# Optimization experiments

Hardware: AMD Instinct MI355X
Metric: run time of the kernel (lower is better)

The kernel has to match this reference:

```python
import jax, jax.numpy as jnp
import numpy as np

D_MODEL = 1024
N_HEADS = 16
D_H = D_MODEL // N_HEADS
B, S = 2, 2048


def setup_inputs() -> dict:
    key = jax.random.key(0)
    ks = jax.random.split(key, 12)
    s = 1.0 / np.sqrt(D_MODEL)
    inp = {
        "Q": jax.random.normal(ks[0], (B, S, D_MODEL), jnp.float32),
        "K": jax.random.normal(ks[1], (B, S, D_MODEL), jnp.float32),
        "V": jax.random.normal(ks[2], (B, S, D_MODEL), jnp.float32),
        # causal mask: True means masked out (matches masked_fill semantics)
        "masked": jnp.broadcast_to(~jnp.tril(jnp.ones((S, S), bool)), (B, S, S)),
        "WQ_w": jax.random.uniform(ks[3], (D_MODEL, D_MODEL), jnp.float32, -s, s),
        "WQ_b": jax.random.uniform(ks[4], (D_MODEL,), jnp.float32, -s, s),
        "WK_w": jax.random.uniform(ks[5], (D_MODEL, D_MODEL), jnp.float32, -s, s),
        "WK_b": jax.random.uniform(ks[6], (D_MODEL,), jnp.float32, -s, s),
        "WV_w": jax.random.uniform(ks[7], (D_MODEL, D_MODEL), jnp.float32, -s, s),
        "WV_b": jax.random.uniform(ks[8], (D_MODEL,), jnp.float32, -s, s),
        "Wo_w": jax.random.uniform(ks[9], (D_MODEL, D_MODEL), jnp.float32, -s, s),
        "Wo_b": jax.random.uniform(ks[10], (D_MODEL,), jnp.float32, -s, s),
    }
    return inp


def reference(Q, K, V, masked, WQ_w, WQ_b, WK_w, WK_b, WV_w, WV_b, Wo_w, Wo_b):
    b = Q.shape[0]
    # torch Linear: y = x @ W^T + b
    def split_heads(x):
        return x.reshape(b, -1, N_HEADS, D_H).transpose(0, 2, 1, 3)  # [B,H,S,d_h]

    q = split_heads(Q @ WQ_w.T + WQ_b)
    k = split_heads(K @ WK_w.T + WK_b)
    v = split_heads(V @ WV_w.T + WV_b)

    scores = jnp.einsum("bhqd,bhkd->bhqk", q, k) / np.sqrt(D_H)
    scores = jnp.where(masked[:, None, :, :], jnp.float32(-1e9), scores)
    attn = jax.nn.softmax(scores, axis=-1)
    ctx = jnp.einsum("bhqk,bhkd->bhqd", attn, v)  # [B,H,S,d_h]
    ctx = ctx.transpose(0, 2, 1, 3).reshape(b, -1, N_HEADS * D_H)
    return ctx @ Wo_w.T + Wo_b
```

## Files before the change

kernel.cpp:

```cpp
#include <hip/hip_runtime.h>
#include <hip/hip_bf16.h>
#include <math.h>


typedef __bf16 bf16_t;
typedef bf16_t bf16x8 __attribute__((ext_vector_type(8)));
typedef bf16_t bf16x4 __attribute__((ext_vector_type(4)));
typedef float f32x4 __attribute__((ext_vector_type(4)));

#define MFMA16(a, b, c) __builtin_amdgcn_mfma_f32_16x16x32_bf16(a, b, c, 0, 0, 0)

constexpr int S_LEN = 2048;
constexpr int DMODEL = 1024;
constexpr int DHEAD = 64;
constexpr int MTOT = 2 * S_LEN;
constexpr size_t NQ = (size_t)MTOT * DMODEL;
constexpr size_t NW = (size_t)DMODEL * DMODEL;
constexpr float ESC = 0.18033688011112042f;

__device__ __forceinline__ void load_lds16(const void* g, void* l) {
  __builtin_amdgcn_global_load_lds((const __attribute__((address_space(1))) void*)g,
                                   (__attribute__((address_space(3))) void*)l, 16, 0, 0);
}

__device__ __forceinline__ void swap32(unsigned& a, unsigned& b) {
#if __has_builtin(__builtin_amdgcn_permlane32_swap)
  auto r = __builtin_amdgcn_permlane32_swap(a, b, false, false);
  a = r[0]; b = r[1];
#else
  asm volatile("s_nop 1\n\tv_permlane32_swap_b32 %0, %1\n\ts_nop 1"
               : "+v"(a), "+v"(b));
#endif
}
__device__ __forceinline__ void swap16(unsigned& a, unsigned& b) {
#if __has_builtin(__builtin_amdgcn_permlane16_swap)
  auto r = __builtin_amdgcn_permlane16_swap(a, b, false, false);
  a = r[0]; b = r[1];
#else
  asm volatile("s_nop 1\n\tv_permlane16_swap_b32 %0, %1\n\ts_nop 1"
               : "+v"(a), "+v"(b));
#endif
}

__device__ __forceinline__ float fexp2(float x) {
#if __has_builtin(__builtin_amdgcn_exp2f)
  return __builtin_amdgcn_exp2f(x);
#else
  float r;
  asm("v_exp_f32 %0, %1\n\ts_nop 1" : "=v"(r) : "v"(x));
  return r;
#endif
}

__global__ __launch_bounds__(256) void convert_w(
    const float* __restrict__ W0, const float* __restrict__ W1,
    const float* __restrict__ W2, const float* __restrict__ W3,
    bf16_t* __restrict__ dst) {
  const size_t i = ((size_t)blockIdx.x * 256 + threadIdx.x) * 4;
  const float* s;
  size_t off = i;
  if (off < NW) { s = W0; }
  else if (off < 2 * NW) { s = W1; off -= NW; }
  else if (off < 3 * NW) { s = W2; off -= 2 * NW; }
  else { s = W3; off -= 3 * NW; }
  const float4 v4 = *(const float4*)(s + off);
  bf16x4 b;
  b[0] = (bf16_t)v4.x; b[1] = (bf16_t)v4.y; b[2] = (bf16_t)v4.z; b[3] = (bf16_t)v4.w;
  *(bf16x4*)(dst + i) = b;
}

__global__ __launch_bounds__(256, 3) void gemm_qkv(const float* __restrict__ Qf,
                                                   const float* __restrict__ Kf,
                                                   const float* __restrict__ Vf,
                                                   const bf16_t* __restrict__ Wbase,
                                                   const float* __restrict__ b0,
                                                   const float* __restrict__ b1,
                                                   const float* __restrict__ b2,
                                                   bf16_t* __restrict__ obase) {
  __shared__ bf16_t As[128 * 64];
  __shared__ bf16_t Ws[128 * 64];
  const int z = blockIdx.z;
  const int bm = blockIdx.x * 128, bn = blockIdx.y * 128;
  const int lane = threadIdx.x & 63, wave = threadIdx.x >> 6;
  const int col = lane & 15, quad = lane >> 4;
  const int wm = (wave >> 1) * 64, wn = (wave & 1) * 64;
  const int srow8 = lane >> 3, g8 = (lane & 7) ^ srow8;

  f32x4 acc[4][4];
#pragma unroll
  for (int i = 0; i < 4; i++)
#pragma unroll
    for (int j = 0; j < 4; j++)
#pragma unroll
      for (int r = 0; r < 4; r++) acc[i][j][r] = 0.f;

  const float* Af = ((z == 0) ? Qf : (z == 1) ? Kf : Vf) + (size_t)bm * 1024;
  const bf16_t* Wb = Wbase + z * NW + (size_t)bn * 1024;
  const float* bias = (z == 0) ? b0 : ((z == 1) ? b1 : b2);
  bf16_t* out = obase + z * NQ;

  f32x4 pre[8];
  auto grloadA = [&](int k0) {
#pragma unroll
    for (int i = 0; i < 4; i++) {
      const int rbase = (i * 4 + wave) * 8;
      const float* src = Af + (size_t)(rbase + srow8) * 1024 + k0 + g8 * 8;
      pre[2 * i] = *(const f32x4*)src;
      pre[2 * i + 1] = *(const f32x4*)(src + 4);
    }
  };

  grloadA(0);
  for (int k0 = 0; k0 < 1024; k0 += 64) {
    __syncthreads();
#pragma unroll
    for (int i = 0; i < 4; i++) {
      const int rbase = (i * 4 + wave) * 8;
      bf16x8 pk;
#pragma unroll
      for (int j = 0; j < 4; j++) {
        pk[j] = (bf16_t)pre[2 * i][j];
        pk[4 + j] = (bf16_t)pre[2 * i + 1][j];
      }
      *(bf16x8*)&As[rbase * 64 + lane * 8] = pk;
      load_lds16(Wb + (size_t)(rbase + srow8) * 1024 + k0 + g8 * 8, Ws + rbase * 64);
    }
    __syncthreads();
    if (k0 + 64 < 1024) grloadA(k0 + 64);
#pragma unroll
    for (int kc = 0; kc < 2; kc++) {
      const int slot = (kc * 4 + quad) ^ (col & 7);
      bf16x8 af[4], wf[4];
#pragma unroll
      for (int i = 0; i < 4; i++) af[i] = *(const bf16x8*)&As[(wm + i * 16 + col) * 64 + slot * 8];
#pragma unroll
      for (int j = 0; j < 4; j++) wf[j] = *(const bf16x8*)&Ws[(wn + j * 16 + col) * 64 + slot * 8];
#pragma unroll
      for (int i = 0; i < 4; i++)
#pragma unroll
        for (int j = 0; j < 4; j++) acc[i][j] = MFMA16(af[i], wf[j], acc[i][j]);
    }
  }

  const float esc = (z == 0) ? ESC : 1.0f;
#pragma unroll
  for (int i = 0; i < 4; i++) {
#pragma unroll
    for (int j = 0; j < 4; j++) {
      const int n = bn + wn + j * 16 + col;
      const float bv = bias[n];
      const int h = n >> 6, dh = n & 63;
      if (z < 2) {
#pragma unroll
        for (int r = 0; r < 4; r++) {
          const int m = bm + wm + i * 16 + quad * 4 + r;
          const int b = m >> 11, s = m & 2047;
          out[((size_t)((b * 16 + h) * S_LEN + s) << 6) | dh] =
              (bf16_t)((acc[i][j][r] + bv) * esc);
        }
      } else {
        const int m0 = bm + wm + i * 16 + quad * 4;
        const int b = m0 >> 11, s0 = m0 & 2047;
        bf16x4 p4;
#pragma unroll
        for (int r = 0; r < 4; r++) p4[r] = (bf16_t)(acc[i][j][r] + bv);
        *(bf16x4*)&out[(((size_t)((b * 16 + h) * DHEAD + dh)) << 11) | s0] = p4;
      }
    }
  }
}

__global__ __launch_bounds__(256, 2) void gemm_out(const bf16_t* __restrict__ A,
                                                   const float* __restrict__ pO,
                                                   const float* __restrict__ pL,
                                                   const bf16_t* __restrict__ W,
                                                   const float* __restrict__ bias,
                                                   float* __restrict__ out) {
  __shared__ bf16_t As[64 * 64];
  __shared__ bf16_t Ws[128 * 64];
  const int bm = blockIdx.x * 64, bn = blockIdx.y * 128;
  const int lane = threadIdx.x & 63, wave = threadIdx.x >> 6;
  const int col = lane & 15, quad = lane >> 4;
  const int wm = (wave >> 1) * 32, wn = (wave & 1) * 64;
  const int srow = lane >> 3, s7 = lane & 7;
  const int g = s7 ^ srow;

  const int tq = (bm >> 7) & 15;
  const bool isB = (tq >= 8);
  const int p = isB ? (15 - tq) : tq;
  const int b = bm >> 11;
  const int lr0 = (0 * 4 + wave) * 8 + srow;
  const int lr1 = (1 * 4 + wave) * 8 + srow;
  const int rt0 = (bm & 64) + lr0;
  const int rt1 = (bm & 64) + lr1;

  f32x4 acc[2][4];
#pragma unroll
  for (int i = 0; i < 2; i++)
#pragma unroll
    for (int j = 0; j < 4; j++)
#pragma unroll
      for (int r = 0; r < 4; r++) acc[i][j][r] = 0.f;

  const bf16_t* Ab = A + (size_t)bm * 1024;
  const bf16_t* Wb = W + (size_t)bn * 1024;

  f32x4 preO[8];
  float preL[4];
  auto grloadO = [&](int k0) {
    const int h = k0 >> 6;
    const int pair = (b * 16 + h) * 8 + p;
    const float* O0 = pO + (size_t)(pair * 2 + 0) * (128 * 64);
    const float* O1 = pO + (size_t)(pair * 2 + 1) * (128 * 64);
    const float* L0 = pL + (pair * 2 + 0) * 128;
    const float* L1 = pL + (pair * 2 + 1) * 128;
    preO[0] = *(const f32x4*)&O0[rt0 * 64 + g * 8];
    preO[1] = *(const f32x4*)&O0[rt0 * 64 + g * 8 + 4];
    preO[2] = *(const f32x4*)&O1[rt0 * 64 + g * 8];
    preO[3] = *(const f32x4*)&O1[rt0 * 64 + g * 8 + 4];
    preO[4] = *(const f32x4*)&O0[rt1 * 64 + g * 8];
    preO[5] = *(const f32x4*)&O0[rt1 * 64 + g * 8 + 4];
    preO[6] = *(const f32x4*)&O1[rt1 * 64 + g * 8];
    preO[7] = *(const f32x4*)&O1[rt1 * 64 + g * 8 + 4];
    preL[0] = L0[rt0]; preL[1] = L1[rt0];
    preL[2] = L0[rt1]; preL[3] = L1[rt1];
  };
  auto writeAB = [&]() {
#pragma unroll
    for (int i = 0; i < 2; i++) {
      const float inv = 1.f / (preL[2 * i] + preL[2 * i + 1]);
      bf16x8 pk;
#pragma unroll
      for (int j = 0; j < 4; j++) {
        pk[j] = (bf16_t)((preO[4 * i][j] + preO[4 * i + 2][j]) * inv);
        pk[4 + j] = (bf16_t)((preO[4 * i + 1][j] + preO[4 * i + 3][j]) * inv);
      }
      *(bf16x8*)&As[(i * 4 + wave) * 8 * 64 + lane * 8] = pk;
    }
  };

  if (isB) grloadO(0);
  for (int k0 = 0; k0 < 1024; k0 += 64) {
    __syncthreads();
    if (isB) {
      writeAB();
    } else {
#pragma unroll
      for (int i = 0; i < 2; i++) {
        const int rbase = (i * 4 + wave) * 8;
        load_lds16(Ab + (size_t)(rbase + srow) * 1024 + k0 + g * 8, As + rbase * 64);
      }
    }
#pragma unroll
    for (int i = 0; i < 4; i++) {
      const int rbase = (i * 4 + wave) * 8;
      load_lds16(Wb + (size_t)(rbase + srow) * 1024 + k0 + g * 8, Ws + rbase * 64);
    }
    __syncthreads();
    if (isB && k0 + 64 < 1024) grloadO(k0 + 64);
#pragma unroll
    for (int kc = 0; kc < 2; kc++) {
      const int slot = (kc * 4 + quad) ^ (col & 7);
      bf16x8 af[2], wf[4];
#pragma unroll
      for (int i = 0; i < 2; i++) af[i] = *(const bf16x8*)&As[(wm + i * 16 + col) * 64 + slot * 8];
#pragma unroll
      for (int j = 0; j < 4; j++) wf[j] = *(const bf16x8*)&Ws[(wn + j * 16 + col) * 64 + slot * 8];
#pragma unroll
      for (int i = 0; i < 2; i++)
#pragma unroll
        for (int j = 0; j < 4; j++) acc[i][j] = MFMA16(af[i], wf[j], acc[i][j]);
    }
  }

#pragma unroll
  for (int i = 0; i < 2; i++)
#pragma unroll
    for (int j = 0; j < 4; j++) {
      const int n = bn + wn + j * 16 + col;
      const float bv = bias[n];
#pragma unroll
      for (int r = 0; r < 4; r++) {
        const int m = bm + wm + i * 16 + quad * 4 + r;
        out[(size_t)m * DMODEL + n] = acc[i][j][r] + bv;
      }
    }
}

__global__ __launch_bounds__(256, 2) void attn(const bf16_t* __restrict__ q,
                                               const bf16_t* __restrict__ k,
                                               const bf16_t* __restrict__ vT,
                                               bf16_t* __restrict__ ctx,
                                               float* __restrict__ pO,
                                               float* __restrict__ pL) {
  const int bh = blockIdx.x;
  const int p = blockIdx.y;
  const int s = blockIdx.z;
  const int tB = 15 - p;
  const int nA = s ? 0 : (2 * p + 2);
  const int cB0 = s ? (15 - 2 * p) : 0;
  const int lane = threadIdx.x & 63, wave = threadIdx.x >> 6;
  const int col = lane & 15, quad = lane >> 4;
  const int qrel = wave * 16 + col;

  __shared__ bf16_t Ks[2][64 * 64];
  __shared__ bf16_t Vs[2][64 * 64];

  const bf16_t* kbh = k + (size_t)bh * S_LEN * DHEAD;
  const bf16_t* vbh = vT + (size_t)bh * DHEAD * S_LEN;

  const int srow8 = lane >> 3, s7 = lane & 7;
  const int g8 = s7 ^ srow8;

  auto stage = [&](int c, int b) {
#pragma unroll
    for (int i = 0; i < 2; i++) {
      const int rbase = (i * 4 + wave) * 8;
      load_lds16(kbh + (size_t)(c * 64 + rbase + srow8) * DHEAD + g8 * 8,
                 &Ks[b][rbase * 64]);
    }
#pragma unroll
    for (int i = 0; i < 2; i++) {
      const int dbase = (i * 4 + wave) * 8;
      load_lds16(vbh + (size_t)(dbase + srow8) * S_LEN + c * 64 + g8 * 8,
                 &Vs[b][dbase * 64]);
    }
  };

  bf16x8 aqw[2][2];
  f32x4 o0[4], o1[4], lacc0, lacc1;
  const f32x4 Zv = {0.f, 0.f, 0.f, 0.f};

  auto setup = [&](int tile_) {
    const int tq = tile_ ? tB : p;
    const bf16_t* qb = q + ((size_t)bh * S_LEN + tq * 128 + qrel) * DHEAD;
    aqw[0][0] = *(const bf16x8*)(qb + quad * 8);
    aqw[0][1] = *(const bf16x8*)(qb + 32 + quad * 8);
    aqw[1][0] = *(const bf16x8*)(qb + (size_t)64 * DHEAD + quad * 8);
    aqw[1][1] = *(const bf16x8*)(qb + (size_t)64 * DHEAD + 32 + quad * 8);
#pragma unroll
    for (int r = 0; r < 4; r++) { lacc0[r] = 0.f; lacc1[r] = 0.f; }
#pragma unroll
    for (int db = 0; db < 4; db++)
#pragma unroll
      for (int r = 0; r < 4; r++) { o0[db][r] = 0.f; o1[db][r] = 0.f; }
  };

  auto expw = [&](const f32x4& sv, int nb, bool dmask, f32x4& lac,
                  unsigned& w0, unsigned& w1) {
    union { bf16x4 v; unsigned u[2]; } pw;
#pragma unroll
    for (int r = 0; r < 4; r++) {
      float pv = fexp2(sv[r]);
      if (dmask && (nb * 16 + quad * 4 + r) > qrel) pv = 0.f;
      lac[r] += pv;
      pw.v[r] = (bf16_t)pv;
    }
    w0 = pw.u[0]; w1 = pw.u[1];
  };

  stage(cB0, 0);
  int buf = 0;

#pragma unroll 1
  for (int i = 0; i < 17; ++i) {
    const bool inB = (i >= nA);
    const int c = inB ? (cB0 + i - nA) : i;
    const int cm = inB ? (2 * tB + 1) : (2 * p + 1);

    if (i == 0) setup(inB ? 1 : 0);
    else if (i == nA) setup(1);

    __syncthreads();

    if (i < 16) {
      const int i1 = i + 1;
      const int c1 = (i1 < nA) ? i1 : (cB0 + i1 - nA);
      stage(c1, buf ^ 1);
    }

    const bool skip0 = (c == cm);
    const bool mask0 = (c == cm - 1);
    const bool mask1 = (c == cm);

    f32x4 s0[4], s1[4];
    {
      const int sl = quad ^ (col & 7);
      bf16x8 kf[4];
#pragma unroll
      for (int nb = 0; nb < 4; nb++)
        kf[nb] = *(const bf16x8*)&Ks[buf][(nb * 16 + col) * 64 + sl * 8];
      __builtin_amdgcn_s_setprio(1);
      if (!skip0) {
#pragma unroll
        for (int nb = 0; nb < 4; nb++) s0[nb] = MFMA16(kf[nb], aqw[0][0], Zv);
      }
#pragma unroll
      for (int nb = 0; nb < 4; nb++) s1[nb] = MFMA16(kf[nb], aqw[1][0], Zv);
      __builtin_amdgcn_s_setprio(0);
    }
    {
      const int sl = (4 + quad) ^ (col & 7);
      bf16x8 kf[4];
#pragma unroll
      for (int nb = 0; nb < 4; nb++)
        kf[nb] = *(const bf16x8*)&Ks[buf][(nb * 16 + col) * 64 + sl * 8];
      __builtin_amdgcn_s_setprio(1);
      if (!skip0) {
#pragma unroll
        for (int nb = 0; nb < 4; nb++) s0[nb] = MFMA16(kf[nb], aqw[0][1], s0[nb]);
      }
#pragma unroll
      for (int nb = 0; nb < 4; nb++) s1[nb] = MFMA16(kf[nb], aqw[1][1], s1[nb]);
      __builtin_amdgcn_s_setprio(0);
    }

#pragma unroll
    for (int kcp = 0; kcp < 2; kcp++) {
      const int sl = (kcp * 4 + quad) ^ (col & 7);
      bf16x8 bv[4];
#pragma unroll
      for (int db = 0; db < 4; db++)
        bv[db] = *(const bf16x8*)&Vs[buf][(db * 16 + col) * 64 + sl * 8];

      union { unsigned u[4]; bf16x8 v; } pa1, pa0;
      {
        unsigned X0, X1, Y0, Y1;
        expw(s1[2 * kcp], 2 * kcp, mask1, lacc1, X0, X1);
        expw(s1[2 * kcp + 1], 2 * kcp + 1, mask1, lacc1, Y0, Y1);
        swap32(X0, Y0); swap16(X0, Y0);
        swap32(X1, Y1); swap16(X1, Y1);
        pa1.u[0] = X0; pa1.u[1] = X1; pa1.u[2] = Y0; pa1.u[3] = Y1;
      }
      if (!skip0) {
        unsigned X0, X1, Y0, Y1;
        expw(s0[2 * kcp], 2 * kcp, mask0, lacc0, X0, X1);
        expw(s0[2 * kcp + 1], 2 * kcp + 1, mask0, lacc0, Y0, Y1);
        swap32(X0, Y0); swap16(X0, Y0);
        swap32(X1, Y1); swap16(X1, Y1);
        pa0.u[0] = X0; pa0.u[1] = X1; pa0.u[2] = Y0; pa0.u[3] = Y1;
      }
      __builtin_amdgcn_s_setprio(1);
      if (!skip0) {
#pragma unroll
        for (int db = 0; db < 4; db++) o0[db] = MFMA16(bv[db], pa0.v, o0[db]);
      }
#pragma unroll
      for (int db = 0; db < 4; db++) o1[db] = MFMA16(bv[db], pa1.v, o1[db]);
      __builtin_amdgcn_s_setprio(0);
    }

    if (i == nA - 1) {
      float l0 = lacc0[0] + lacc0[1] + lacc0[2] + lacc0[3];
      l0 += __shfl_xor(l0, 16); l0 += __shfl_xor(l0, 32);
      float l1 = lacc1[0] + lacc1[1] + lacc1[2] + lacc1[3];
      l1 += __shfl_xor(l1, 16); l1 += __shfl_xor(l1, 32);
      const float inv0 = 1.f / l0, inv1 = 1.f / l1;
      const int b = bh >> 4, h = bh & 15;
      bf16_t* cb0 = ctx + ((size_t)(b * S_LEN + p * 128 + qrel)) * DMODEL + h * DHEAD;
      bf16_t* cb1 = cb0 + (size_t)64 * DMODEL;
#pragma unroll
      for (int db = 0; db < 4; db++) {
        bf16x4 w0, w1;
#pragma unroll
        for (int r = 0; r < 4; r++) {
          w0[r] = (bf16_t)(o0[db][r] * inv0);
          w1[r] = (bf16_t)(o1[db][r] * inv1);
        }
        *(bf16x4*)&cb0[db * 16 + quad * 4] = w0;
        *(bf16x4*)&cb1[db * 16 + quad * 4] = w1;
      }
    }
    buf ^= 1;
  }

  float l0 = lacc0[0] + lacc0[1] + lacc0[2] + lacc0[3];
  l0 += __shfl_xor(l0, 16); l0 += __shfl_xor(l0, 32);
  float l1 = lacc1[0] + lacc1[1] + lacc1[2] + lacc1[3];
  l1 += __shfl_xor(l1, 16); l1 += __shfl_xor(l1, 32);
  const int slot = ((bh * 8 + p) << 1) | s;
  float* myO = pO + (size_t)slot * (128 * 64);
  float* myL = pL + slot * 128;
#pragma unroll
  for (int db = 0; db < 4; db++) {
    *(f32x4*)&myO[(size_t)qrel * 64 + db * 16 + quad * 4] = o0[db];
    *(f32x4*)&myO[(size_t)(64 + qrel) * 64 + db * 16 + quad * 4] = o1[db];
  }
  if (quad == 0) { myL[qrel] = l0; myL[64 + qrel] = l1; }
}

extern "C" void kernel_launch(void* const* d_in, const int* in_sizes, int n_in,
                              void* d_out, int out_size, void* d_ws, size_t ws_size,
                              hipStream_t stream) {
  const float* Q = (const float*)d_in[0];
  const float* K = (const float*)d_in[1];
  const float* V = (const float*)d_in[2];
  const float* WQw = (const float*)d_in[4];
  const float* WQb = (const float*)d_in[5];
  const float* WKw = (const float*)d_in[6];
  const float* WKb = (const float*)d_in[7];
  const float* WVw = (const float*)d_in[8];
  const float* WVb = (const float*)d_in[9];
  const float* Wow = (const float*)d_in[10];
  const float* Wob = (const float*)d_in[11];

  bf16_t* base = (bf16_t*)d_ws;
  bf16_t* Wc = base + 3 * NQ;
  bf16_t* qp = base + 3 * NQ + 4 * NW;
  bf16_t* ctx = base;
  float* pO = (float*)(base + NQ);
  float* pL = (float*)(Wc + NW / 2);

  convert_w<<<dim3((unsigned)(4 * NW / 4 / 256)), dim3(256), 0, stream>>>(
      WQw, WKw, WVw, Wow, Wc);

  gemm_qkv<<<dim3(32, 8, 3), dim3(256), 0, stream>>>(Q, K, V, Wc, WQb, WKb, WVb, qp);
  attn<<<dim3(32, 8, 2), dim3(256), 0, stream>>>(qp, qp + NQ, qp + 2 * NQ, ctx, pO, pL);
  gemm_out<<<dim3(64, 8), dim3(256), 0, stream>>>(ctx, pO, pL, Wc + 3 * NW, Wob,
                                                  (float*)d_out);
}
```

Baseline: 225.7 us.

## Fuse fp32-to-bf16 weight conversion into GEMM loaders, drop convert kernel

Removes the separate convert_w kernel and has gemm_qkv and gemm_out load fp32 weights directly, converting them to bf16 in registers before writing to LDS. This cuts one kernel launch and the extra write and read of the bf16 weight copy. In exchange, each GEMM block reads fp32 weights (twice the bytes) and repeats the conversion, and the async global-to-LDS path for W becomes register staging with more VGPR pressure. It also adds s_setprio around the MFMA bursts.

```diff
diff --git a/kernel.cpp b/kernel.cpp
--- a/kernel.cpp
+++ b/kernel.cpp
@@ -52,27 +52,12 @@
 #endif
 }
 
-__global__ __launch_bounds__(256) void convert_w(
-    const float* __restrict__ W0, const float* __restrict__ W1,
-    const float* __restrict__ W2, const float* __restrict__ W3,
-    bf16_t* __restrict__ dst) {
-  const size_t i = ((size_t)blockIdx.x * 256 + threadIdx.x) * 4;
-  const float* s;
-  size_t off = i;
-  if (off < NW) { s = W0; }
-  else if (off < 2 * NW) { s = W1; off -= NW; }
-  else if (off < 3 * NW) { s = W2; off -= 2 * NW; }
-  else { s = W3; off -= 3 * NW; }
-  const float4 v4 = *(const float4*)(s + off);
-  bf16x4 b;
-  b[0] = (bf16_t)v4.x; b[1] = (bf16_t)v4.y; b[2] = (bf16_t)v4.z; b[3] = (bf16_t)v4.w;
-  *(bf16x4*)(dst + i) = b;
-}
-
 __global__ __launch_bounds__(256, 3) void gemm_qkv(const float* __restrict__ Qf,
                                                    const float* __restrict__ Kf,
                                                    const float* __restrict__ Vf,
-                                                   const bf16_t* __restrict__ Wbase,
+                                                   const float* __restrict__ W0,
+                                                   const float* __restrict__ W1,
+                                                   const float* __restrict__ W2,
                                                    const float* __restrict__ b0,
                                                    const float* __restrict__ b1,
                                                    const float* __restrict__ b2,
@@ -95,38 +80,46 @@
       for (int r = 0; r < 4; r++) acc[i][j][r] = 0.f;
 
   const float* Af = ((z == 0) ? Qf : (z == 1) ? Kf : Vf) + (size_t)bm * 1024;
-  const bf16_t* Wb = Wbase + z * NW + (size_t)bn * 1024;
+  const float* Wf = ((z == 0) ? W0 : (z == 1) ? W1 : W2) + (size_t)bn * 1024;
   const float* bias = (z == 0) ? b0 : ((z == 1) ? b1 : b2);
   bf16_t* out = obase + z * NQ;
 
-  f32x4 pre[8];
-  auto grloadA = [&](int k0) {
+  f32x4 preA[8], preW[8];
+  auto grload = [&](int k0) {
 #pragma unroll
     for (int i = 0; i < 4; i++) {
       const int rbase = (i * 4 + wave) * 8;
-      const float* src = Af + (size_t)(rbase + srow8) * 1024 + k0 + g8 * 8;
-      pre[2 * i] = *(const f32x4*)src;
-      pre[2 * i + 1] = *(const f32x4*)(src + 4);
-    }
-  };
-
-  grloadA(0);
+      const float* sa = Af + (size_t)(rbase + srow8) * 1024 + k0 + g8 * 8;
+      const float* sw = Wf + (size_t)(rbase + srow8) * 1024 + k0 + g8 * 8;
+      preA[2 * i] = *(const f32x4*)sa;
+      preA[2 * i + 1] = *(const f32x4*)(sa + 4);
+      preW[2 * i] = *(const f32x4*)sw;
+      preW[2 * i + 1] = *(const f32x4*)(sw + 4);
+    }
+  };
+  auto writeAW = [&]() {
+#pragma unroll
+    for (int i = 0; i < 4; i++) {
+      const int rbase = (i * 4 + wave) * 8;
+      bf16x8 pa, pw;
+#pragma unroll
+      for (int j = 0; j < 4; j++) {
+        pa[j] = (bf16_t)preA[2 * i][j];
+        pa[4 + j] = (bf16_t)preA[2 * i + 1][j];
+        pw[j] = (bf16_t)preW[2 * i][j];
+        pw[4 + j] = (bf16_t)preW[2 * i + 1][j];
+      }
+      *(bf16x8*)&As[rbase * 64 + lane * 8] = pa;
+      *(bf16x8*)&Ws[rbase * 64 + lane * 8] = pw;
+    }
+  };
+
+  grload(0);
   for (int k0 = 0; k0 < 1024; k0 += 64) {
     __syncthreads();
-#pragma unroll
-    for (int i = 0; i < 4; i++) {
-      const int rbase = (i * 4 + wave) * 8;
-      bf16x8 pk;
-#pragma unroll
-      for (int j = 0; j < 4; j++) {
-        pk[j] = (bf16_t)pre[2 * i][j];
-        pk[4 + j] = (bf16_t)pre[2 * i + 1][j];
-      }
-      *(bf16x8*)&As[rbase * 64 + lane * 8] = pk;
-      load_lds16(Wb + (size_t)(rbase + srow8) * 1024 + k0 + g8 * 8, Ws + rbase * 64);
-    }
+    writeAW();
     __syncthreads();
-    if (k0 + 64 < 1024) grloadA(k0 + 64);
+    if (k0 + 64 < 1024) grload(k0 + 64);
 #pragma unroll
     for (int kc = 0; kc < 2; kc++) {
       const int slot = (kc * 4 + quad) ^ (col & 7);
@@ -135,10 +128,12 @@
       for (int i = 0; i < 4; i++) af[i] = *(const bf16x8*)&As[(wm + i * 16 + col) * 64 + slot * 8];
 #pragma unroll
       for (int j = 0; j < 4; j++) wf[j] = *(const bf16x8*)&Ws[(wn + j * 16 + col) * 64 + slot * 8];
+      __builtin_amdgcn_s_setprio(1);
 #pragma unroll
       for (int i = 0; i < 4; i++)
 #pragma unroll
         for (int j = 0; j < 4; j++) acc[i][j] = MFMA16(af[i], wf[j], acc[i][j]);
+      __builtin_amdgcn_s_setprio(0);
     }
   }
 
@@ -173,7 +168,7 @@
 __global__ __launch_bounds__(256, 2) void gemm_out(const bf16_t* __restrict__ A,
                                                    const float* __restrict__ pO,
                                                    const float* __restrict__ pL,
-                                                   const bf16_t* __restrict__ W,
+                                                   const float* __restrict__ Wf,
                                                    const float* __restrict__ bias,
                                                    float* __restrict__ out) {
   __shared__ bf16_t As[64 * 64];
@@ -203,10 +198,28 @@
       for (int r = 0; r < 4; r++) acc[i][j][r] = 0.f;
 
   const bf16_t* Ab = A + (size_t)bm * 1024;
-  const bf16_t* Wb = W + (size_t)bn * 1024;
-
+  const float* Wb = Wf + (size_t)bn * 1024;
+
+  bf16x8 preA[2];
+  f32x4 preW[8];
   f32x4 preO[8];
   float preL[4];
+  auto grloadA = [&](int k0) {
+#pragma unroll
+    for (int i = 0; i < 2; i++) {
+      const int rbase = (i * 4 + wave) * 8;
+      preA[i] = *(const bf16x8*)(Ab + (size_t)(rbase + srow) * 1024 + k0 + g * 8);
+    }
+  };
+  auto grloadW = [&](int k0) {
+#pragma unroll
+    for (int i = 0; i < 4; i++) {
+      const int rbase = (i * 4 + wave) * 8;
+      const float* sw = Wb + (size_t)(rbase + srow) * 1024 + k0 + g * 8;
+      preW[2 * i] = *(const f32x4*)sw;
+      preW[2 * i + 1] = *(const f32x4*)(sw + 4);
+    }
+  };
   auto grloadO = [&](int k0) {
     const int h = k0 >> 6;
     const int pair = (b * 16 + h) * 8 + p;
@@ -225,6 +238,11 @@
     preL[0] = L0[rt0]; preL[1] = L1[rt0];
     preL[2] = L0[rt1]; preL[3] = L1[rt1];
   };
+  auto writeA = [&]() {
+#pragma unroll
+    for (int i = 0; i < 2; i++)
+      *(bf16x8*)&As[(i * 4 + wave) * 8 * 64 + lane * 8] = preA[i];
+  };
   auto writeAB = [&]() {
 #pragma unroll
     for (int i = 0; i < 2; i++) {
@@ -238,26 +256,31 @@
       *(bf16x8*)&As[(i * 4 + wave) * 8 * 64 + lane * 8] = pk;
     }
   };
-
-  if (isB) grloadO(0);
+  auto writeW = [&]() {
+#pragma unroll
+    for (int i = 0; i < 4; i++) {
+      const int rbase = (i * 4 + wave) * 8;
+      bf16x8 pw;
+#pragma unroll
+      for (int j = 0; j < 4; j++) {
+        pw[j] = (bf16_t)preW[2 * i][j];
+        pw[4 + j] = (bf16_t)preW[2 * i + 1][j];
+      }
+      *(bf16x8*)&Ws[rbase * 64 + lane * 8] = pw;
+    }
+  };
+
+  if (isB) grloadO(0); else grloadA(0);
+  grloadW(0);
   for (int k0 = 0; k0 < 1024; k0 += 64) {
     __syncthreads();
-    if (isB) {
-      writeAB();
-    } else {
-#pragma unroll
-      for (int i = 0; i < 2; i++) {
-        const int rbase = (i * 4 + wave) * 8;
-        load_lds16(Ab + (size_t)(rbase + srow) * 1024 + k0 + g * 8, As + rbase * 64);
-      }
-    }
-#pragma unroll
-    for (int i = 0; i < 4; i++) {
-      const int rbase = (i * 4 + wave) * 8;
-      load_lds16(Wb + (size_t)(rbase + srow) * 1024 + k0 + g * 8, Ws + rbase * 64);
-    }
+    if (isB) writeAB(); else writeA();
+    writeW();
     __syncthreads();
-    if (isB && k0 + 64 < 1024) grloadO(k0 + 64);
+    if (k0 + 64 < 1024) {
+      if (isB) grloadO(k0 + 64); else grloadA(k0 + 64);
+      grloadW(k0 + 64);
+    }
 #pragma unroll
     for (int kc = 0; kc < 2; kc++) {
       const int slot = (kc * 4 + quad) ^ (col & 7);
@@ -266,10 +289,12 @@
       for (int i = 0; i < 2; i++) af[i] = *(const bf16x8*)&As[(wm + i * 16 + col) * 64 + slot * 8];
 #pragma unroll
       for (int j = 0; j < 4; j++) wf[j] = *(const bf16x8*)&Ws[(wn + j * 16 + col) * 64 + slot * 8];
+      __builtin_amdgcn_s_setprio(1);
 #pragma unroll
       for (int i = 0; i < 2; i++)
 #pragma unroll
         for (int j = 0; j < 4; j++) acc[i][j] = MFMA16(af[i], wf[j], acc[i][j]);
+      __builtin_amdgcn_s_setprio(0);
     }
   }
 
@@ -511,11 +536,9 @@
   float* pO = (float*)(base + NQ);
   float* pL = (float*)(Wc + NW / 2);
 
-  convert_w<<<dim3((unsigned)(4 * NW / 4 / 256)), dim3(256), 0, stream>>>(
-      WQw, WKw, WVw, Wow, Wc);
-
-  gemm_qkv<<<dim3(32, 8, 3), dim3(256), 0, stream>>>(Q, K, V, Wc, WQb, WKb, WVb, qp);
+  gemm_qkv<<<dim3(32, 8, 3), dim3(256), 0, stream>>>(Q, K, V, WQw, WKw, WVw,
+                                                     WQb, WKb, WVb, qp);
   attn<<<dim3(32, 8, 2), dim3(256), 0, stream>>>(qp, qp + NQ, qp + 2 * NQ, ctx, pO, pL);
-  gemm_out<<<dim3(64, 8), dim3(256), 0, stream>>>(ctx, pO, pL, Wc + 3 * NW, Wob,
+  gemm_out<<<dim3(64, 8), dim3(256), 0, stream>>>(ctx, pO, pL, Wow, Wob,
                                                   (float*)d_out);
 }
```

After: 315.8 us. 1.4x slower.
